# Kernel optimization log

Measured on AMD Instinct MI355X. Metric: run time of the kernel, lower is better.

Reference implementation:

```python
import jax, jax.numpy as jnp
import numpy as np

N_NODES = 50000
N_EDGES = 800000
D = 64
H = 128


def setup_inputs() -> dict:
    key = jax.random.key(0)
    ks = jax.random.split(key, 6)
    x = jax.random.normal(ks[0], (N_NODES, D), dtype=jnp.float32)
    edge_index = jax.random.randint(ks[1], (2, N_EDGES), 0, N_NODES, dtype=jnp.int64)
    # GIN MLP params (Linear(D->H) -> ReLU -> Linear(H->D))
    W1 = jax.random.normal(ks[2], (D, H), dtype=jnp.float32) * (1.0 / np.sqrt(D))
    b1 = jnp.zeros((H,), dtype=jnp.float32)
    W2 = jax.random.normal(ks[3], (H, D), dtype=jnp.float32) * (1.0 / np.sqrt(H))
    b2 = jnp.zeros((D,), dtype=jnp.float32)
    eps = jnp.zeros((1, 1), dtype=jnp.float32)  # trainable eps parameter
    return {"x": x, "W1": W1, "b1": b1, "W2": W2, "b2": b2, "eps": eps,
            "edge_index": edge_index}


def reference(x, W1, b1, W2, b2, eps, edge_index):
    src, dst = edge_index[0], edge_index[1]
    # node -> edge gather (0th-order ptensor on each edge = sum of endpoint feats)
    msg = x[src] + x[dst]                                    # [E, D]
    # edge -> node gather: each node sums messages of its incident edges
    agg = (jax.ops.segment_sum(msg, src, num_segments=N_NODES)
           + jax.ops.segment_sum(msg, dst, num_segments=N_NODES))  # [N, D]
    ones = jnp.ones((N_EDGES,), dtype=x.dtype)
    deg = (jax.ops.segment_sum(ones, src, num_segments=N_NODES)
           + jax.ops.segment_sum(ones, dst, num_segments=N_NODES))  # [N]
    # subtract deg*x so aggregation reduces to the plain neighbor sum (GIN)
    neighbor = agg - x * deg[:, None]
    out = (1.0 + eps) * x + neighbor                          # eps is [1,1], broadcasts
    # GIN MLP
    h = jax.nn.relu(out @ W1 + b1)
    return h @ W2 + b2
```

## Files before the change

### kernel.cpp

```cpp
#include <hip/hip_runtime.h>


#define D 64
#define H 128
#define MPW 8
#define REGSH 6
#define REGSZ 64
#define P1_BLOCKS 256
#define P1_THREADS 1024
#define EVBUF_SZ 6400
#define NR_MAX 1024
#define NCAP 96
#define PSTR 68

typedef __attribute__((ext_vector_type(8))) short short8;
typedef __attribute__((ext_vector_type(4))) float float4v;

__device__ __forceinline__ float lane_bcast(float v, int l) {
    return __uint_as_float(__builtin_amdgcn_readlane(__float_as_uint(v), l));
}

__device__ __forceinline__ unsigned short f2bf(float f) {
    unsigned int u = __float_as_uint(f);
    u = (u + (((u >> 16) & 1u) + 0x7fffu)) >> 16;
    return (unsigned short)u;
}

__device__ __forceinline__ void bf2_acc(unsigned int u, float& a, float& b) {
    a += __uint_as_float(u << 16);
    b += __uint_as_float(u & 0xffff0000u);
}

__global__ void zero_int_kernel(int* __restrict__ p, int n) {
    int i = blockIdx.x * blockDim.x + threadIdx.x;
    if (i < n) p[i] = 0;
}

__global__ void zero_f_kernel(float* __restrict__ p, int n) {
    int i = blockIdx.x * blockDim.x + threadIdx.x;
    if (i < n) p[i] = 0.0f;
}

__global__ void prep_kernel(const float* __restrict__ x,
                            unsigned int* __restrict__ xh2, int npairs,
                            int* __restrict__ cursor, int NR, int CAPB,
                            const float* __restrict__ W1,
                            const float* __restrict__ W2,
                            unsigned short* __restrict__ wsW1,
                            unsigned short* __restrict__ wsW2) {
    int i = blockIdx.x * blockDim.x + threadIdx.x;
    int gs = gridDim.x * blockDim.x;
    for (int k = i; k < npairs; k += gs) {
        float2 v = *(const float2*)(x + (size_t)k * 2);
        unsigned int a = __float_as_uint(v.x);
        unsigned int b = __float_as_uint(v.y);
        a = (a + (((a >> 16) & 1u) + 0x7fffu)) >> 16;
        b = (b + (((b >> 16) & 1u) + 0x7fffu)) >> 16;
        xh2[k] = a | (b << 16);
    }
    if (i < NR) cursor[i] = i * CAPB;
    if (i < 32) xh2[npairs + i] = 0;
    if (i < 8192) {
        int j = i & 7, ln = (i >> 3) & 63;
        int q = (ln >> 4) & 3;
        int tt1 = (i >> 9) & 7, s1 = i >> 12;
        wsW1[i] = f2bf(W1[(s1 * 32 + q * 8 + j) * H + tt1 * 16 + (ln & 15)]);
        int tt2 = (i >> 9) & 3, s2 = i >> 11;
        wsW2[i] = f2bf(W2[(s2 * 32 + q * 8 + j) * D + tt2 * 16 + (ln & 15)]);
    }
}

__global__ __launch_bounds__(P1_THREADS) void part1_kernel(
    const int* __restrict__ src, const int* __restrict__ dst,
    int* __restrict__ cursor, unsigned int* __restrict__ evarr,
    int E, int N, int NR, int CAPB, int EPB)
{
    __shared__ unsigned int evbuf[EVBUF_SZ];
    __shared__ unsigned int sortbuf[EVBUF_SZ];
    __shared__ unsigned short tickbuf[EVBUF_SZ];
    __shared__ int hist[NR_MAX];
    __shared__ int lbase[NR_MAX];
    __shared__ int gbase[NR_MAX];
    __shared__ int scanw[P1_THREADS];
    int t = threadIdx.x;

    for (int b = t; b < NR; b += P1_THREADS) hist[b] = 0;
    __syncthreads();

    int e0 = blockIdx.x * EPB;
    int ne = E - e0; if (ne > EPB) ne = EPB; if (ne < 0) ne = 0;
    for (int i = t; i < ne; i += P1_THREADS) {
        int s = src[e0 + i], d = dst[e0 + i];
        s = (s < 0) ? 0 : ((s >= N) ? N - 1 : s);
        d = (d < 0) ? 0 : ((d >= N) ? N - 1 : d);
        unsigned int ev0 = ((unsigned int)s << 16) | (unsigned int)d;
        unsigned int ev1 = ((unsigned int)d << 16) | (unsigned int)s;
        int k0 = atomicAdd(&hist[s >> REGSH], 1);
        int k1 = atomicAdd(&hist[d >> REGSH], 1);
        evbuf[2 * i]     = ev0; tickbuf[2 * i]     = (unsigned short)k0;
        evbuf[2 * i + 1] = ev1; tickbuf[2 * i + 1] = (unsigned short)k1;
    }
    __syncthreads();

    {
        int h0 = (t < NR) ? hist[t] : 0;
        scanw[t] = h0;
        __syncthreads();
        for (int off = 1; off < P1_THREADS; off <<= 1) {
            int u = (t >= off) ? scanw[t - off] : 0;
            __syncthreads();
            scanw[t] += u;
            __syncthreads();
        }
        if (t < NR) lbase[t] = scanw[t] - h0;
    }

    for (int b = t; b < NR; b += P1_THREADS) {
        int c = hist[b];
        gbase[b] = c ? atomicAdd(&cursor[b], c) : 0;
    }
    __syncthreads();

    int nev = 2 * ne;
    for (int i = t; i < nev; i += P1_THREADS) {
        unsigned int ev = evbuf[i];
        int reg = (int)(ev >> (16 + REGSH));
        sortbuf[lbase[reg] + (int)tickbuf[i]] = ev;
    }
    __syncthreads();

    for (int i = t; i < nev; i += P1_THREADS) {
        unsigned int ev = sortbuf[i];
        int reg = (int)(ev >> (16 + REGSH));
        int addr = gbase[reg] + (i - lbase[reg]);
        if (addr < (reg + 1) * CAPB) evarr[addr] = ev;
    }
}

__global__ __launch_bounds__(512, 8) void part2_fused(
    const unsigned int* __restrict__ evarr, const int* __restrict__ cursor,
    const unsigned short* __restrict__ xh, const float* __restrict__ x,
    const float* __restrict__ epsp,
    const unsigned short* __restrict__ wsW1,
    const unsigned short* __restrict__ wsW2,
    const float* __restrict__ b1, const float* __restrict__ b2,
    float* __restrict__ y, int N, int CAPB)
{
    __shared__ unsigned short nbuf[REGSZ * NCAP + 32];
    __shared__ int scnt[REGSZ];
    __shared__ float pre_lds[REGSZ * PSTR];
    int t = threadIdx.x;
    int b = blockIdx.x;
    if (t < REGSZ) scnt[t] = 0;
    __syncthreads();

    int base = b * CAPB;
    int count = cursor[b] - base;
    if (count < 0) count = 0;
    if (count > CAPB) count = CAPB;

    for (int i = t; i < count; i += 512) {
        unsigned int ev = evarr[base + i];
        int row = (int)((ev >> 16) & (REGSZ - 1));
        int k = atomicAdd(&scnt[row], 1);
        if (k < NCAP) nbuf[row * NCAP + k] = (unsigned short)(ev & 0xffffu);
    }
    __syncthreads();

    int wave = t >> 6, lane = t & 63;
    int r = lane >> 5;
    int h = lane & 31;
    float e1 = 1.0f + epsp[0];

    for (int k = 0; k < 8; ++k) {
        int n = wave * 8 + k;
        int v = b * REGSZ + n;
        int m = (v < N) ? scnt[n] : 0;
        m = (m > NCAP) ? NCAP : m;
        float f0 = 0.0f, f1 = 0.0f;
        for (int j = 0; j < m; j += 32) {
            int cc[16];
#pragma unroll
            for (int q = 0; q < 16; ++q) {
                int ii = j + 2 * q + r;
                int c = (int)nbuf[n * NCAP + ii];
                cc[q] = (ii < m) ? c : N;
            }
            unsigned int u[16];
#pragma unroll
            for (int q = 0; q < 16; ++q)
                u[q] = *(const unsigned int*)(xh + (size_t)cc[q] * D + 2 * h);
#pragma unroll
            for (int q = 0; q < 16; ++q) bf2_acc(u[q], f0, f1);
        }
        f0 += __shfl_xor(f0, 32, 64);
        f1 += __shfl_xor(f1, 32, 64);
        if (r == 0) {
            float2 sv = make_float2(0.0f, 0.0f);
            if (v < N) sv = *(const float2*)(x + (size_t)v * D + 2 * h);
            pre_lds[n * PSTR + 2 * h]     = f0 + e1 * sv.x;
            pre_lds[n * PSTR + 2 * h + 1] = f1 + e1 * sv.y;
        }
    }
    __syncthreads();

    int p = wave >> 1, hh = wave & 1;
    int quad = lane >> 4, lm = lane & 15;
    int row0 = p * 16 + lm;

    short8 a1f[2];
#pragma unroll
    for (int s = 0; s < 2; ++s) {
        const float* rp = &pre_lds[row0 * PSTR + s * 32 + quad * 8];
        float4v p0 = *(const float4v*)rp;
        float4v p1 = *(const float4v*)(rp + 4);
        short8 a;
        a[0] = (short)f2bf(p0[0]); a[1] = (short)f2bf(p0[1]);
        a[2] = (short)f2bf(p0[2]); a[3] = (short)f2bf(p0[3]);
        a[4] = (short)f2bf(p1[0]); a[5] = (short)f2bf(p1[1]);
        a[6] = (short)f2bf(p1[2]); a[7] = (short)f2bf(p1[3]);
        a1f[s] = a;
    }
    __syncthreads();

    unsigned short* hbuf = (unsigned short*)pre_lds;

    float4v acc1[4];
#pragma unroll
    for (int i = 0; i < 4; ++i) {
        int tt = hh * 4 + i;
        float bb = b1[tt * 16 + lm];
        float4v c = {bb, bb, bb, bb};
#pragma unroll
        for (int s = 0; s < 2; ++s) {
            short8 bw = *(const short8*)&wsW1[((s * 8 + tt) * 64 + lane) * 8];
            c = __builtin_amdgcn_mfma_f32_16x16x32_bf16(a1f[s], bw, c, 0, 0, 0);
        }
        acc1[i] = c;
    }

    unsigned short* hb = &hbuf[p * 16 * H];
#pragma unroll
    for (int i = 0; i < 4; ++i) {
        int tt = hh * 4 + i;
#pragma unroll
        for (int rr = 0; rr < 4; ++rr) {
            float hv = fmaxf(acc1[i][rr], 0.0f);
            hb[(quad * 4 + rr) * H + tt * 16 + lm] = f2bf(hv);
        }
    }
    __syncthreads();

    short8 a2[4];
#pragma unroll
    for (int s = 0; s < 4; ++s)
        a2[s] = *(const short8*)&hb[lm * H + s * 32 + quad * 8];

    int v0t = b * REGSZ + p * 16;
#pragma unroll
    for (int i = 0; i < 2; ++i) {
        int tt = hh * 2 + i;
        float bb = b2[tt * 16 + lm];
        float4v c = {bb, bb, bb, bb};
#pragma unroll
        for (int s = 0; s < 4; ++s) {
            short8 bw = *(const short8*)&wsW2[((s * 4 + tt) * 64 + lane) * 8];
            c = __builtin_amdgcn_mfma_f32_16x16x32_bf16(a2[s], bw, c, 0, 0, 0);
        }
#pragma unroll
        for (int rr = 0; rr < 4; ++rr) {
            int v = v0t + quad * 4 + rr;
            if (v < N) y[(size_t)v * D + tt * 16 + lm] = c[rr];
        }
    }
}


__global__ void count_kernel(const int* __restrict__ ei, int* __restrict__ deg,
                             int twoE, int N) {
    int i = blockIdx.x * blockDim.x + threadIdx.x;
    if (i < twoE) {
        int v = ei[i];
        v = (v < 0) ? 0 : ((v >= N) ? N - 1 : v);
        atomicAdd(&deg[v], 1);
    }
}

__global__ __launch_bounds__(256) void scan_part1(const int* __restrict__ deg,
                                                  int* __restrict__ bsum, int n) {
    __shared__ int red[256];
    int t = threadIdx.x;
    int i = blockIdx.x * 256 + t;
    red[t] = (i < n) ? deg[i] : 0;
    __syncthreads();
    for (int off = 128; off > 0; off >>= 1) {
        if (t < off) red[t] += red[t + off];
        __syncthreads();
    }
    if (t == 0) bsum[blockIdx.x] = red[0];
}

__global__ __launch_bounds__(256) void scan_part2(const int* __restrict__ bsum,
                                                  int* __restrict__ boff,
                                                  int* __restrict__ rowstart_n, int nb) {
    __shared__ int s[256];
    int t = threadIdx.x;
    int v = (t < nb) ? bsum[t] : 0;
    s[t] = v;
    __syncthreads();
    for (int off = 1; off < 256; off <<= 1) {
        int u = (t >= off) ? s[t - off] : 0;
        __syncthreads();
        s[t] += u;
        __syncthreads();
    }
    if (t < nb) boff[t] = s[t] - v;
    if (t == 255) *rowstart_n = s[255];
}

__global__ __launch_bounds__(256) void scan_part3(const int* __restrict__ deg,
                                                  const int* __restrict__ boff,
                                                  int* __restrict__ rowstart,
                                                  int* __restrict__ cursor, int n) {
    __shared__ int s[256];
    int t = threadIdx.x;
    int i = blockIdx.x * 256 + t;
    int v = (i < n) ? deg[i] : 0;
    s[t] = v;
    __syncthreads();
    for (int off = 1; off < 256; off <<= 1) {
        int u = (t >= off) ? s[t - off] : 0;
        __syncthreads();
        s[t] += u;
        __syncthreads();
    }
    if (i < n) {
        int r = boff[blockIdx.x] + s[t] - v;
        rowstart[i] = r;
        cursor[i] = r;
    }
}

__global__ __launch_bounds__(256) void scan_single(const int* __restrict__ deg,
                                                   int* __restrict__ rowstart,
                                                   int* __restrict__ cursor,
                                                   int n, int chunk) {
    __shared__ int psum[256];
    int t = threadIdx.x;
    int lo = t * chunk;
    int hi = lo + chunk; if (hi > n) hi = n;
    int s = 0;
    for (int i = lo; i < hi; ++i) s += deg[i];
    psum[t] = s;
    __syncthreads();
    for (int off = 1; off < 256; off <<= 1) {
        int v = (t >= off) ? psum[t - off] : 0;
        __syncthreads();
        psum[t] += v;
        __syncthreads();
    }
    int run = (t == 0) ? 0 : psum[t - 1];
    for (int i = lo; i < hi; ++i) {
        int d = deg[i];
        rowstart[i] = run;
        cursor[i] = run;
        run += d;
    }
    if (t == 255) rowstart[n] = psum[255];
}

__global__ __launch_bounds__(256) void fill_xcd(
    const int* __restrict__ src, const int* __restrict__ dst,
    int* __restrict__ cursor, int* __restrict__ col,
    int E, int N, int npg)
{
    int grp = blockIdx.x & 7;
    int slice = blockIdx.x >> 3;
    int lo = grp * npg;
    int hi = lo + npg; if (hi > N) hi = N;
    int stride = (gridDim.x >> 3) * 256;
    for (int i = slice * 256 + threadIdx.x; i < E; i += stride) {
        int s = src[i], d = dst[i];
        s = (s < 0) ? 0 : ((s >= N) ? N - 1 : s);
        d = (d < 0) ? 0 : ((d >= N) ? N - 1 : d);
        if (s >= lo && s < hi) { int p = atomicAdd(&cursor[s], 1); col[p] = d; }
        if (d >= lo && d < hi) { int q = atomicAdd(&cursor[d], 1); col[q] = s; }
    }
}

__global__ __launch_bounds__(256) void gather_csr2(
    const float* __restrict__ x, const float* __restrict__ epsp,
    const int* __restrict__ rowstart, const int* __restrict__ col,
    float* __restrict__ pre, int N)
{
    int wid = (blockIdx.x * 256 + threadIdx.x) >> 6;
    int lane = threadIdx.x & 63;
    int v0 = wid * 2;
    if (v0 >= N) return;
    int v1 = v0 + 1;
    float eps1 = 1.0f + epsp[0];
    int j0 = rowstart[v0], re0 = rowstart[v0 + 1];
    float a0 = eps1 * x[(size_t)v0 * D + lane];
    int j1 = 0, re1 = 0;
    float a1 = 0.0f;
    if (v1 < N) {
        j1 = rowstart[v1]; re1 = rowstart[v1 + 1];
        a1 = eps1 * x[(size_t)v1 * D + lane];
    }
    while (j0 + 8 <= re0 && j1 + 8 <= re1) {
        float p0 = x[(size_t)col[j0 + 0] * D + lane];
        float p1 = x[(size_t)col[j0 + 1] * D + lane];
        float p2 = x[(size_t)col[j0 + 2] * D + lane];
        float p3 = x[(size_t)col[j0 + 3] * D + lane];
        float p4 = x[(size_t)col[j0 + 4] * D + lane];
        float p5 = x[(size_t)col[j0 + 5] * D + lane];
        float p6 = x[(size_t)col[j0 + 6] * D + lane];
        float p7 = x[(size_t)col[j0 + 7] * D + lane];
        float q0 = x[(size_t)col[j1 + 0] * D + lane];
        float q1 = x[(size_t)col[j1 + 1] * D + lane];
        float q2 = x[(size_t)col[j1 + 2] * D + lane];
        float q3 = x[(size_t)col[j1 + 3] * D + lane];
        float q4 = x[(size_t)col[j1 + 4] * D + lane];
        float q5 = x[(size_t)col[j1 + 5] * D + lane];
        float q6 = x[(size_t)col[j1 + 6] * D + lane];
        float q7 = x[(size_t)col[j1 + 7] * D + lane];
        a0 += ((p0 + p1) + (p2 + p3)) + ((p4 + p5) + (p6 + p7));
        a1 += ((q0 + q1) + (q2 + q3)) + ((q4 + q5) + (q6 + q7));
        j0 += 8; j1 += 8;
    }
    for (; j0 + 8 <= re0; j0 += 8) {
        float p0 = x[(size_t)col[j0 + 0] * D + lane];
        float p1 = x[(size_t)col[j0 + 1] * D + lane];
        float p2 = x[(size_t)col[j0 + 2] * D + lane];
        float p3 = x[(size_t)col[j0 + 3] * D + lane];
        float p4 = x[(size_t)col[j0 + 4] * D + lane];
        float p5 = x[(size_t)col[j0 + 5] * D + lane];
        float p6 = x[(size_t)col[j0 + 6] * D + lane];
        float p7 = x[(size_t)col[j0 + 7] * D + lane];
        a0 += ((p0 + p1) + (p2 + p3)) + ((p4 + p5) + (p6 + p7));
    }
    for (; j1 + 8 <= re1; j1 += 8) {
        float q0 = x[(size_t)col[j1 + 0] * D + lane];
        float q1 = x[(size_t)col[j1 + 1] * D + lane];
        float q2 = x[(size_t)col[j1 + 2] * D + lane];
        float q3 = x[(size_t)col[j1 + 3] * D + lane];
        float q4 = x[(size_t)col[j1 + 4] * D + lane];
        float q5 = x[(size_t)col[j1 + 5] * D + lane];
        float q6 = x[(size_t)col[j1 + 6] * D + lane];
        float q7 = x[(size_t)col[j1 + 7] * D + lane];
        a1 += ((q0 + q1) + (q2 + q3)) + ((q4 + q5) + (q6 + q7));
    }
    for (; j0 < re0; ++j0) a0 += x[(size_t)col[j0] * D + lane];
    for (; j1 < re1; ++j1) a1 += x[(size_t)col[j1] * D + lane];
    pre[(size_t)v0 * D + lane] = a0;
    if (v1 < N) pre[(size_t)v1 * D + lane] = a1;
}

__device__ __forceinline__ void mlp_store(
    const float* acc, float* sW, int v0, int t, int lane, int nNodes,
    const float* __restrict__ W2,
    const float* __restrict__ b1, const float* __restrict__ b2,
    float* __restrict__ y)
{
    float b1a = b1[lane], b1b = b1[lane + 64];
    float ha[MPW], hb[MPW];
#pragma unroll
    for (int m = 0; m < MPW; ++m) { ha[m] = b1a; hb[m] = b1b; }
#pragma unroll 4
    for (int f = 0; f < D; ++f) {
        float wa = sW[f * H + lane];
        float wb = sW[f * H + lane + 64];
#pragma unroll
        for (int m = 0; m < MPW; ++m) {
            float o = lane_bcast(acc[m], f);
            ha[m] += o * wa;
            hb[m] += o * wb;
        }
    }
#pragma unroll
    for (int m = 0; m < MPW; ++m) {
        ha[m] = fmaxf(ha[m], 0.0f);
        hb[m] = fmaxf(hb[m], 0.0f);
    }

    __syncthreads();
    for (int i = t; i < H * D; i += 256) sW[i] = W2[i];
    __syncthreads();

    float b2v = b2[lane];
    float yv[MPW];
#pragma unroll
    for (int m = 0; m < MPW; ++m) yv[m] = b2v;
#pragma unroll 4
    for (int k = 0; k < 64; ++k) {
        float w = sW[k * D + lane];
#pragma unroll
        for (int m = 0; m < MPW; ++m) yv[m] += lane_bcast(ha[m], k) * w;
    }
#pragma unroll 4
    for (int k = 0; k < 64; ++k) {
        float w = sW[(k + 64) * D + lane];
#pragma unroll
        for (int m = 0; m < MPW; ++m) yv[m] += lane_bcast(hb[m], k) * w;
    }
#pragma unroll
    for (int m = 0; m < MPW; ++m) {
        int v = v0 + m;
        if (v < nNodes) y[(size_t)v * D + lane] = yv[m];
    }
}

__global__ __launch_bounds__(256) void mlp_pre(
    const float* __restrict__ pre, const float* __restrict__ W1,
    const float* __restrict__ b1, const float* __restrict__ W2,
    const float* __restrict__ b2, float* __restrict__ y, int nNodes)
{
    __shared__ float sW[D * H];
    int t = threadIdx.x;
    for (int i = t; i < D * H; i += 256) sW[i] = W1[i];
    __syncthreads();
    int wave = t >> 6, lane = t & 63;
    int v0 = (blockIdx.x * 4 + wave) * MPW;
    float acc[MPW];
#pragma unroll
    for (int m = 0; m < MPW; ++m) {
        int v = v0 + m;
        acc[m] = (v < nNodes) ? pre[(size_t)v * D + lane] : 0.0f;
    }
    mlp_store(acc, sW, v0, t, lane, nNodes, W2, b1, b2, y);
}

__global__ __launch_bounds__(256) void gather_mlp_csr(
    const float* __restrict__ x, const float* __restrict__ W1,
    const float* __restrict__ b1, const float* __restrict__ W2,
    const float* __restrict__ b2, const float* __restrict__ epsp,
    const int* __restrict__ rowstart, const int* __restrict__ col,
    float* __restrict__ y, int nNodes)
{
    __shared__ float sW[D * H];
    int t = threadIdx.x;
    for (int i = t; i < D * H; i += 256) sW[i] = W1[i];
    __syncthreads();
    int wave = t >> 6, lane = t & 63;
    float eps1 = 1.0f + epsp[0];
    int v0 = (blockIdx.x * 4 + wave) * MPW;
    float acc[MPW];
#pragma unroll
    for (int m = 0; m < MPW; ++m) {
        int v = v0 + m;
        float a = 0.0f;
        if (v < nNodes) {
            int rs = rowstart[v], re = rowstart[v + 1];
            a = eps1 * x[(size_t)v * D + lane];
            int j = rs;
            for (; j + 8 <= re; j += 8) {
                float p0 = x[(size_t)col[j + 0] * D + lane];
                float p1 = x[(size_t)col[j + 1] * D + lane];
                float p2 = x[(size_t)col[j + 2] * D + lane];
                float p3 = x[(size_t)col[j + 3] * D + lane];
                float p4 = x[(size_t)col[j + 4] * D + lane];
                float p5 = x[(size_t)col[j + 5] * D + lane];
                float p6 = x[(size_t)col[j + 6] * D + lane];
                float p7 = x[(size_t)col[j + 7] * D + lane];
                a += ((p0 + p1) + (p2 + p3)) + ((p4 + p5) + (p6 + p7));
            }
            for (; j < re; ++j) a += x[(size_t)col[j] * D + lane];
        }
        acc[m] = a;
    }
    mlp_store(acc, sW, v0, t, lane, nNodes, W2, b1, b2, y);
}

__global__ void scatter_kernel(const float* __restrict__ x,
                               const int* __restrict__ src,
                               const int* __restrict__ dst,
                               float* __restrict__ agg, int E, int N)
{
    int tid = blockIdx.x * blockDim.x + threadIdx.x;
    int e = tid >> 6, lane = tid & 63;
    if (e < E) {
        int s = src[e], d = dst[e];
        s = (s < 0) ? 0 : ((s >= N) ? N - 1 : s);
        d = (d < 0) ? 0 : ((d >= N) ? N - 1 : d);
        float xs = x[(size_t)s * D + lane];
        float xd = x[(size_t)d * D + lane];
        atomicAdd(&agg[(size_t)s * D + lane], xd);
        atomicAdd(&agg[(size_t)d * D + lane], xs);
    }
}

__global__ __launch_bounds__(256) void mlp_from_agg(
    const float* __restrict__ x, const float* __restrict__ W1,
    const float* __restrict__ b1, const float* __restrict__ W2,
    const float* __restrict__ b2, const float* __restrict__ epsp,
    float* __restrict__ yio, int nNodes)
{
    __shared__ float sW[D * H];
    int t = threadIdx.x;
    for (int i = t; i < D * H; i += 256) sW[i] = W1[i];
    __syncthreads();
    int wave = t >> 6, lane = t & 63;
    float eps1 = 1.0f + epsp[0];
    int v0 = (blockIdx.x * 4 + wave) * MPW;
    float acc[MPW];
#pragma unroll
    for (int m = 0; m < MPW; ++m) {
        int v = v0 + m;
        acc[m] = (v < nNodes)
                   ? (eps1 * x[(size_t)v * D + lane] + yio[(size_t)v * D + lane])
                   : 0.0f;
    }
    mlp_store(acc, sW, v0, t, lane, nNodes, W2, b1, b2, yio);
}

extern "C" void kernel_launch(void* const* d_in, const int* in_sizes, int n_in,
                              void* d_out, int out_size, void* d_ws, size_t ws_size,
                              hipStream_t stream)
{
    const float* x   = (const float*)d_in[0];
    const float* W1  = (const float*)d_in[1];
    const float* b1  = (const float*)d_in[2];
    const float* W2  = (const float*)d_in[3];
    const float* b2  = (const float*)d_in[4];
    const float* eps = (const float*)d_in[5];
    const int*   ei  = (const int*)d_in[6];
    float* out = (float*)d_out;

    int N = in_sizes[0] / D;
    int E = in_sizes[6] / 2;
    const int* src = ei;
    const int* dst = ei + E;

    int nb = (N + 255) / 256;

    int NR = (N + REGSZ - 1) >> REGSH;
    int meanE = (NR > 0) ? (2 * E + NR - 1) / NR : 0;
    int CAPB = meanE + meanE / 4 + 128;
    int EPB = (E + P1_BLOCKS - 1) / P1_BLOCKS;
    size_t off_cur  = 0;
    size_t off_ev   = (off_cur + (size_t)NR * 4 + 15) & ~(size_t)15;
    size_t off_xh   = (off_ev + (size_t)NR * CAPB * 4 + 15) & ~(size_t)15;
    size_t off_w1   = (off_xh + (size_t)(N + 1) * D * 2 + 15) & ~(size_t)15;
    size_t off_w2   = off_w1 + 8192 * 2;
    size_t need_part = off_w2 + 8192 * 2;

    size_t csr_ints = (size_t)(3 * N + 1 + 2 * E) + 512;
    size_t need_csr = csr_ints * sizeof(int);
    size_t need_split = need_csr + (size_t)N * D * sizeof(float);
    int mlp_blocks = (N + 4 * MPW - 1) / (4 * MPW);

    if (ws_size >= need_part && N >= REGSZ && N <= 65535
        && NR <= NR_MAX && 2 * EPB <= EVBUF_SZ && (N * D) % 2 == 0) {
        char* base = (char*)d_ws;
        int*            cursor = (int*)(base + off_cur);
        unsigned int*   evarr  = (unsigned int*)(base + off_ev);
        unsigned short* xh     = (unsigned short*)(base + off_xh);
        unsigned short* wsW1   = (unsigned short*)(base + off_w1);
        unsigned short* wsW2   = (unsigned short*)(base + off_w2);
        int npairs = N * D / 2;

        prep_kernel<<<1024, 256, 0, stream>>>(
            x, (unsigned int*)xh, npairs, cursor, NR, CAPB, W1, W2, wsW1, wsW2);
        part1_kernel<<<P1_BLOCKS, P1_THREADS, 0, stream>>>(
            src, dst, cursor, evarr, E, N, NR, CAPB, EPB);
        part2_fused<<<NR, 512, 0, stream>>>(
            evarr, cursor, xh, x, eps, wsW1, wsW2, b1, b2, out, N, CAPB);
    } else if (ws_size >= need_csr) {
        int*   deg      = (int*)d_ws;
        int*   cursor   = deg + N;
        int*   rowstart = cursor + N;
        int*   col      = rowstart + (N + 1);
        int*   bsum     = col + 2 * E;
        int*   boff     = bsum + 256;
        float* pre      = (float*)(boff + 256);

        zero_int_kernel<<<(N + 255) / 256, 256, 0, stream>>>(deg, N);
        count_kernel<<<(2 * E + 255) / 256, 256, 0, stream>>>(ei, deg, 2 * E, N);
        if (nb <= 256) {
            scan_part1<<<nb, 256, 0, stream>>>(deg, bsum, N);
            scan_part2<<<1, 256, 0, stream>>>(bsum, boff, &rowstart[N], nb);
            scan_part3<<<nb, 256, 0, stream>>>(deg, boff, rowstart, cursor, N);
        } else {
            int chunk = (N + 255) / 256;
            scan_single<<<1, 256, 0, stream>>>(deg, rowstart, cursor, N, chunk);
        }
        fill_xcd<<<2048, 256, 0, stream>>>(src, dst, cursor, col, E, N, (N + 7) / 8);
        int waves = (N + 1) / 2;
        int gather_blocks = (waves + 3) / 4;
        if (ws_size >= need_split) {
            gather_csr2<<<gather_blocks, 256, 0, stream>>>(x, eps, rowstart, col, pre, N);
            mlp_pre<<<mlp_blocks, 256, 0, stream>>>(pre, W1, b1, W2, b2, out, N);
        } else {
            gather_mlp_csr<<<mlp_blocks, 256, 0, stream>>>(
                x, W1, b1, W2, b2, eps, rowstart, col, out, N);
        }
    } else {
        int nd = N * D;
        zero_f_kernel<<<(nd + 255) / 256, 256, 0, stream>>>(out, nd);
        long long st = (long long)E * 64;
        scatter_kernel<<<(int)((st + 255) / 256), 256, 0, stream>>>(x, src, dst, out, E, N);
        mlp_from_agg<<<mlp_blocks, 256, 0, stream>>>(x, W1, b1, W2, b2, eps, out, N);
    }
}
```

Baseline: 134.6 us.

## Replace global region cursors with per-block sorted chunks and offset table

The edge-partition kernel no longer reserves space in global per-region buckets with atomics. Each block now writes its locally sorted events as one contiguous chunk, plus a table of per-region offsets. The fused node kernel then has 256 threads each walk one block's segment for its region to build the neighbor lists. This removes the global atomics, the cursor initialization and the bucket-capacity overflow. In exchange, the second kernel's gather becomes short serial, poorly coalesced reads spread across many chunks.

```diff
diff --git a/kernel.cpp b/kernel.cpp
--- a/kernel.cpp
+++ b/kernel.cpp
@@ -43,7 +43,6 @@
 
 __global__ void prep_kernel(const float* __restrict__ x,
                             unsigned int* __restrict__ xh2, int npairs,
-                            int* __restrict__ cursor, int NR, int CAPB,
                             const float* __restrict__ W1,
                             const float* __restrict__ W2,
                             unsigned short* __restrict__ wsW1,
@@ -58,7 +57,6 @@
         b = (b + (((b >> 16) & 1u) + 0x7fffu)) >> 16;
         xh2[k] = a | (b << 16);
     }
-    if (i < NR) cursor[i] = i * CAPB;
     if (i < 32) xh2[npairs + i] = 0;
     if (i < 8192) {
         int j = i & 7, ln = (i >> 3) & 63;
@@ -72,15 +70,14 @@
 
 __global__ __launch_bounds__(P1_THREADS) void part1_kernel(
     const int* __restrict__ src, const int* __restrict__ dst,
-    int* __restrict__ cursor, unsigned int* __restrict__ evarr,
-    int E, int N, int NR, int CAPB, int EPB)
+    unsigned int* __restrict__ evarr, int* __restrict__ table,
+    int E, int N, int NR, int CHK, int EPB)
 {
     __shared__ unsigned int evbuf[EVBUF_SZ];
     __shared__ unsigned int sortbuf[EVBUF_SZ];
     __shared__ unsigned short tickbuf[EVBUF_SZ];
     __shared__ int hist[NR_MAX];
     __shared__ int lbase[NR_MAX];
-    __shared__ int gbase[NR_MAX];
     __shared__ int scanw[P1_THREADS];
     int t = threadIdx.x;
 
@@ -114,11 +111,6 @@
         }
         if (t < NR) lbase[t] = scanw[t] - h0;
     }
-
-    for (int b = t; b < NR; b += P1_THREADS) {
-        int c = hist[b];
-        gbase[b] = c ? atomicAdd(&cursor[b], c) : 0;
-    }
     __syncthreads();
 
     int nev = 2 * ne;
@@ -129,41 +121,41 @@
     }
     __syncthreads();
 
-    for (int i = t; i < nev; i += P1_THREADS) {
-        unsigned int ev = sortbuf[i];
-        int reg = (int)(ev >> (16 + REGSH));
-        int addr = gbase[reg] + (i - lbase[reg]);
-        if (addr < (reg + 1) * CAPB) evarr[addr] = ev;
-    }
+    int brow = blockIdx.x * (NR + 1);
+    for (int i = t; i < NR; i += P1_THREADS) table[brow + i] = lbase[i];
+    if (t == 0) table[brow + NR] = nev;
+    size_t cbase = (size_t)blockIdx.x * CHK;
+    for (int i = t; i < nev; i += P1_THREADS) evarr[cbase + i] = sortbuf[i];
 }
 
 __global__ __launch_bounds__(512, 8) void part2_fused(
-    const unsigned int* __restrict__ evarr, const int* __restrict__ cursor,
+    const unsigned int* __restrict__ evarr, const int* __restrict__ table,
     const unsigned short* __restrict__ xh, const float* __restrict__ x,
     const float* __restrict__ epsp,
     const unsigned short* __restrict__ wsW1,
     const unsigned short* __restrict__ wsW2,
     const float* __restrict__ b1, const float* __restrict__ b2,
-    float* __restrict__ y, int N, int CAPB)
+    float* __restrict__ y, int N, int CHK, int NR)
 {
     __shared__ unsigned short nbuf[REGSZ * NCAP + 32];
     __shared__ int scnt[REGSZ];
     __shared__ float pre_lds[REGSZ * PSTR];
     int t = threadIdx.x;
-    int b = blockIdx.x;
+    int breg = blockIdx.x;
     if (t < REGSZ) scnt[t] = 0;
     __syncthreads();
 
-    int base = b * CAPB;
-    int count = cursor[b] - base;
-    if (count < 0) count = 0;
-    if (count > CAPB) count = CAPB;
-
-    for (int i = t; i < count; i += 512) {
-        unsigned int ev = evarr[base + i];
-        int row = (int)((ev >> 16) & (REGSZ - 1));
-        int k = atomicAdd(&scnt[row], 1);
-        if (k < NCAP) nbuf[row * NCAP + k] = (unsigned short)(ev & 0xffffu);
+    if (t < P1_BLOCKS) {
+        int sb = t;
+        int lb = table[sb * (NR + 1) + breg];
+        int le = table[sb * (NR + 1) + breg + 1];
+        const unsigned int* ch = evarr + (size_t)sb * CHK;
+        for (int k = lb; k < le; ++k) {
+            unsigned int ev = ch[k];
+            int row = (int)((ev >> 16) & (REGSZ - 1));
+            int kk = atomicAdd(&scnt[row], 1);
+            if (kk < NCAP) nbuf[row * NCAP + kk] = (unsigned short)(ev & 0xffffu);
+        }
     }
     __syncthreads();
 
@@ -174,7 +166,7 @@
 
     for (int k = 0; k < 8; ++k) {
         int n = wave * 8 + k;
-        int v = b * REGSZ + n;
+        int v = breg * REGSZ + n;
         int m = (v < N) ? scnt[n] : 0;
         m = (m > NCAP) ? NCAP : m;
         float f0 = 0.0f, f1 = 0.0f;
@@ -256,7 +248,7 @@
     for (int s = 0; s < 4; ++s)
         a2[s] = *(const short8*)&hb[lm * H + s * 32 + quad * 8];
 
-    int v0t = b * REGSZ + p * 16;
+    int v0t = breg * REGSZ + p * 16;
 #pragma unroll
     for (int i = 0; i < 2; ++i) {
         int tt = hh * 2 + i;
@@ -634,12 +626,11 @@
     int nb = (N + 255) / 256;
 
     int NR = (N + REGSZ - 1) >> REGSH;
-    int meanE = (NR > 0) ? (2 * E + NR - 1) / NR : 0;
-    int CAPB = meanE + meanE / 4 + 128;
     int EPB = (E + P1_BLOCKS - 1) / P1_BLOCKS;
-    size_t off_cur  = 0;
-    size_t off_ev   = (off_cur + (size_t)NR * 4 + 15) & ~(size_t)15;
-    size_t off_xh   = (off_ev + (size_t)NR * CAPB * 4 + 15) & ~(size_t)15;
+    int CHK = 2 * EPB;
+    size_t off_tab  = 0;
+    size_t off_ev   = (off_tab + (size_t)(NR + 1) * P1_BLOCKS * 4 + 15) & ~(size_t)15;
+    size_t off_xh   = (off_ev + (size_t)P1_BLOCKS * CHK * 4 + 15) & ~(size_t)15;
     size_t off_w1   = (off_xh + (size_t)(N + 1) * D * 2 + 15) & ~(size_t)15;
     size_t off_w2   = off_w1 + 8192 * 2;
     size_t need_part = off_w2 + 8192 * 2;
@@ -652,19 +643,19 @@
     if (ws_size >= need_part && N >= REGSZ && N <= 65535
         && NR <= NR_MAX && 2 * EPB <= EVBUF_SZ && (N * D) % 2 == 0) {
         char* base = (char*)d_ws;
-        int*            cursor = (int*)(base + off_cur);
-        unsigned int*   evarr  = (unsigned int*)(base + off_ev);
-        unsigned short* xh     = (unsigned short*)(base + off_xh);
-        unsigned short* wsW1   = (unsigned short*)(base + off_w1);
-        unsigned short* wsW2   = (unsigned short*)(base + off_w2);
+        int*            table = (int*)(base + off_tab);
+        unsigned int*   evarr = (unsigned int*)(base + off_ev);
+        unsigned short* xh    = (unsigned short*)(base + off_xh);
+        unsigned short* wsW1  = (unsigned short*)(base + off_w1);
+        unsigned short* wsW2  = (unsigned short*)(base + off_w2);
         int npairs = N * D / 2;
 
         prep_kernel<<<1024, 256, 0, stream>>>(
-            x, (unsigned int*)xh, npairs, cursor, NR, CAPB, W1, W2, wsW1, wsW2);
+            x, (unsigned int*)xh, npairs, W1, W2, wsW1, wsW2);
         part1_kernel<<<P1_BLOCKS, P1_THREADS, 0, stream>>>(
-            src, dst, cursor, evarr, E, N, NR, CAPB, EPB);
+            src, dst, evarr, table, E, N, NR, CHK, EPB);
         part2_fused<<<NR, 512, 0, stream>>>(
-            evarr, cursor, xh, x, eps, wsW1, wsW2, b1, b2, out, N, CAPB);
+            evarr, table, xh, x, eps, wsW1, wsW2, b1, b2, out, N, CHK, NR);
     } else if (ws_size >= need_csr) {
         int*   deg      = (int*)d_ws;
         int*   cursor   = deg + N;
```

Measured after the change: 137.5 us. 1.02x slower.
